# Performance work log

Hardware: AMD Instinct MI355X
Metric: run time of the kernel (lower is better)

The kernel has to match this reference:

```python
import jax, jax.numpy as jnp
import numpy as np

B, L, D, H = 2, 2048, 1024, 16
DH = D // H  # per-head dim = 64


def setup_inputs() -> dict:
    key = jax.random.key(0)
    ks = jax.random.split(key, 7)
    s = 1.0 / np.sqrt(D)
    x = jax.random.normal(ks[0], (B, L, D), dtype=jnp.float32)
    Wq = jax.random.normal(ks[1], (D, D), dtype=jnp.float32) * s
    bq = jax.random.normal(ks[2], (D,), dtype=jnp.float32) * s
    Wk = jax.random.normal(ks[3], (D, D), dtype=jnp.float32) * s
    bk = jax.random.normal(ks[4], (D,), dtype=jnp.float32) * s
    Wv = jax.random.normal(ks[5], (D, D), dtype=jnp.float32) * s
    bv = jax.random.normal(ks[6], (D,), dtype=jnp.float32) * s
    # strict upper-triangular causal mask; mask==1 means position is masked (-inf)
    atten_mask = jnp.triu(jnp.ones((L, L), dtype=jnp.int32), k=1)
    return {"x": x, "atten_mask": atten_mask, "Wq": Wq, "bq": bq,
            "Wk": Wk, "bk": bk, "Wv": Wv, "bv": bv}


def reference(x, atten_mask, Wq, bq, Wk, bk, Wv, bv):
    # nn.Linear: y = x @ W^T + b
    q = x @ Wq.T + bq  # [B,L,D]
    k = x @ Wk.T + bk
    v = x @ Wv.T + bv
    # contiguous split into heads == reshape to [B,L,H,DH]
    q = q.reshape(B, L, H, DH)
    k = k.reshape(B, L, H, DH)
    v = v.reshape(B, L, H, DH)
    scale = jnp.sqrt(jnp.float32(DH))
    scores = jnp.einsum('blhd,bmhd->bhlm', q, k) / scale  # [B,H,L,L]
    # torch.where(mask == 1, -inf, scores)
    scores = jnp.where(atten_mask[None, None] == 1, -jnp.inf, scores)
    attn = jax.nn.softmax(scores, axis=-1)
    out = jnp.einsum('bhlm,bmhd->blhd', attn, v)  # [B,L,H,DH]
    return out.reshape(B, L, D)  # concat heads along channel dim
```

## Files before the change

### kernel.cpp

```cpp
#include <hip/hip_runtime.h>
#include <hip/hip_bf16.h>

#define BDIM 2
#define LSEQ 2048
#define DMODEL 1024
#define NH 16
#define DHEAD 64
#define SP 72
#define CTS 136

typedef __bf16 bf16_t;
typedef __attribute__((ext_vector_type(8))) __bf16 bf16x8;
typedef __attribute__((ext_vector_type(4))) __bf16 bf16x4;
typedef __attribute__((ext_vector_type(2))) __bf16 bf16x2;
typedef __attribute__((ext_vector_type(4))) float f32x4;
typedef __attribute__((ext_vector_type(4))) int i32x4;

static __device__ __forceinline__ f32x4 mfma16(bf16x8 a, bf16x8 b, f32x4 c) {
    return __builtin_amdgcn_mfma_f32_16x16x32_bf16(a, b, c, 0, 0, 0);
}

static __device__ __forceinline__ void load_lds16(const bf16_t* g, void* l) {
    __builtin_amdgcn_global_load_lds(
        (const __attribute__((address_space(1))) void*)g,
        (__attribute__((address_space(3))) void*)l, 16, 0, 0);
}

__global__ void convert_all(
    const float* __restrict__ x,
    const float* __restrict__ Wq, const float* __restrict__ Wk, const float* __restrict__ Wv,
    const float* __restrict__ bq, const float* __restrict__ bk, const float* __restrict__ bv,
    bf16_t* __restrict__ cx,
    bf16_t* __restrict__ cWq, bf16_t* __restrict__ cWk, bf16_t* __restrict__ cWv,
    bf16_t* __restrict__ cbq, bf16_t* __restrict__ cbk, bf16_t* __restrict__ cbv,
    float SQ)
{
    const int blk = blockIdx.x;
    const float* src; bf16_t* dst; int base, cnt; float sc = 1.0f;
    if (blk < 1024)      { src = x;  dst = cx;  base = blk * 1024;          cnt = 1024; }
    else if (blk < 1280) { src = Wq; dst = cWq; base = (blk - 1024) * 1024; cnt = 1024; sc = SQ; }
    else if (blk < 1536) { src = Wk; dst = cWk; base = (blk - 1280) * 1024; cnt = 1024; }
    else if (blk < 1792) { src = Wv; dst = cWv; base = (blk - 1536) * 1024; cnt = 1024; }
    else if (blk == 1792){ src = bq; dst = cbq; base = 0; cnt = 256; sc = SQ; }
    else if (blk == 1793){ src = bk; dst = cbk; base = 0; cnt = 256; }
    else                 { src = bv; dst = cbv; base = 0; cnt = 256; }

    for (int i = base + threadIdx.x; i < base + cnt; i += 256) {
        f32x4 v = *(const f32x4*)(src + 4 * (size_t)i);
        bf16x4 o;
        o[0] = (bf16_t)(v[0] * sc); o[1] = (bf16_t)(v[1] * sc);
        o[2] = (bf16_t)(v[2] * sc); o[3] = (bf16_t)(v[3] * sc);
        *(bf16x4*)(dst + 4 * (size_t)i) = o;
    }
}

__global__ __launch_bounds__(512, 2) void qkv_gemm(
    const bf16_t* __restrict__ x,
    const bf16_t* __restrict__ W0, const bf16_t* __restrict__ W1, const bf16_t* __restrict__ W2,
    const bf16_t* __restrict__ b0, const bf16_t* __restrict__ b1, const bf16_t* __restrict__ b2,
    bf16_t* __restrict__ yq, bf16_t* __restrict__ yk, bf16_t* __restrict__ yvT)
{
    __shared__ alignas(16) bf16_t smem[65536];

    const int tid  = threadIdx.x;
    const int lane = tid & 63;
    const int w    = tid >> 6;
    const int quad = lane >> 4;
    const int n16  = lane & 15;
    const int swz  = n16 & 7;
    const int srow = lane >> 3;
    const int schnk = (lane & 7) ^ srow;

    const int s   = blockIdx.x;
    const int sem = ((s & 7) << 3) | (s >> 3);
    const int m0  = (sem >> 2) * 256;
    const int n0  = (sem & 3) * 256;
    const int z   = blockIdx.y;

    const bf16_t* W    = (z == 0) ? W0 : ((z == 1) ? W1 : W2);
    const bf16_t* bias = (z == 0) ? b0 : ((z == 1) ? b1 : b2);

    const int wm = (w >> 2) * 128;
    const int wn = (w & 3) * 64;

    const bf16_t* gA = x + (size_t)(m0 + w * 8 + srow) * DMODEL + schnk * 8;
    const bf16_t* gB = W + (size_t)(n0 + w * 8 + srow) * DMODEL + schnk * 8;

    f32x4 acc[8][4] = {};

    auto stageA = [&](int buf, int h, int kt) {
        bf16_t* d = smem + buf * 32768 + (h * 128 + w * 8) * 64;
        const bf16_t* src = gA + (size_t)(h * 128) * DMODEL + kt * 64;
        load_lds16(src, d);
        load_lds16(src + (size_t)64 * DMODEL, d + 64 * 64);
    };
    auto stageB = [&](int buf, int h, int kt) {
        bf16_t* d = smem + buf * 32768 + 16384 + (h * 128 + w * 8) * 64;
        const bf16_t* src = gB + (size_t)(h * 128) * DMODEL + kt * 64;
        load_lds16(src, d);
        load_lds16(src + (size_t)64 * DMODEL, d + 64 * 64);
    };

    stageA(0, 0, 0); stageA(0, 1, 0);
    stageB(0, 0, 0); stageB(0, 1, 0);
    stageB(1, 0, 1); stageB(1, 1, 1);
    asm volatile("s_waitcnt vmcnt(4)" ::: "memory");
    __builtin_amdgcn_s_barrier();

    for (int u = 0; u < 16; ++u) {
        const int buf = u & 1;
        const bf16_t* Ab = smem + buf * 32768;
        const bf16_t* Bb = Ab + 16384;

        bf16x8 bfr[4][2], af[2][2];
        #pragma unroll
        for (int nt = 0; nt < 4; ++nt) {
            const bf16_t* br = Bb + (wn + nt * 16 + n16) * 64;
            bfr[nt][0] = *(const bf16x8*)(br + ((quad    ) ^ swz) * 8);
            bfr[nt][1] = *(const bf16x8*)(br + ((quad + 4) ^ swz) * 8);
        }
        #pragma unroll
        for (int m2 = 0; m2 < 2; ++m2) {
            const bf16_t* ar = Ab + (wm + m2 * 16 + n16) * 64;
            af[m2][0] = *(const bf16x8*)(ar + ((quad    ) ^ swz) * 8);
            af[m2][1] = *(const bf16x8*)(ar + ((quad + 4) ^ swz) * 8);
        }
        if (u + 1 < 16) stageA(buf ^ 1, 0, u + 1);
        __builtin_amdgcn_s_barrier();
        asm volatile("s_waitcnt lgkmcnt(0)" ::: "memory");
        __builtin_amdgcn_sched_barrier(0);
        __builtin_amdgcn_s_setprio(1);
        #pragma unroll
        for (int m2 = 0; m2 < 2; ++m2)
            #pragma unroll
            for (int nt = 0; nt < 4; ++nt) {
                acc[m2][nt] = mfma16(af[m2][0], bfr[nt][0], acc[m2][nt]);
                acc[m2][nt] = mfma16(af[m2][1], bfr[nt][1], acc[m2][nt]);
            }
        __builtin_amdgcn_s_setprio(0);
        __builtin_amdgcn_s_barrier();

        #pragma unroll
        for (int q = 1; q < 4; ++q) {
            #pragma unroll
            for (int m2 = 0; m2 < 2; ++m2) {
                const bf16_t* ar = Ab + (wm + (2 * q + m2) * 16 + n16) * 64;
                af[m2][0] = *(const bf16x8*)(ar + ((quad    ) ^ swz) * 8);
                af[m2][1] = *(const bf16x8*)(ar + ((quad + 4) ^ swz) * 8);
            }
            if (q == 1) {
                if (u + 1 < 16) stageA(buf ^ 1, 1, u + 1);
                if (u + 2 < 16) stageB(buf, 0, u + 2);
            } else if (q == 2) {
                if (u + 2 < 16) stageB(buf, 1, u + 2);
            }
            __builtin_amdgcn_s_barrier();
            asm volatile("s_waitcnt lgkmcnt(0)" ::: "memory");
            __builtin_amdgcn_sched_barrier(0);
            __builtin_amdgcn_s_setprio(1);
            #pragma unroll
            for (int m2 = 0; m2 < 2; ++m2)
                #pragma unroll
                for (int nt = 0; nt < 4; ++nt) {
                    acc[2 * q + m2][nt] = mfma16(af[m2][0], bfr[nt][0], acc[2 * q + m2][nt]);
                    acc[2 * q + m2][nt] = mfma16(af[m2][1], bfr[nt][1], acc[2 * q + m2][nt]);
                }
            __builtin_amdgcn_s_setprio(0);
            if (q == 3) {
                if (u < 14) asm volatile("s_waitcnt vmcnt(4)" ::: "memory");
                else        asm volatile("s_waitcnt vmcnt(0)" ::: "memory");
            }
            __builtin_amdgcn_s_barrier();
        }
    }

    if (z < 2) {
        bf16_t* y = (z == 0) ? yq : yk;
        bf16_t* Ct = smem;
        #pragma unroll
        for (int hp = 0; hp < 2; ++hp) {
            if (((w & 3) >> 1) == hp) {
                #pragma unroll
                for (int nt = 0; nt < 4; ++nt) {
                    const int jc = (w & 1) * 64 + nt * 16 + n16;
                    const float bv = (float)bias[n0 + hp * 128 + jc];
                    #pragma unroll
                    for (int mt = 0; mt < 8; ++mt) {
                        const int rr = wm + mt * 16 + quad * 4;
                        #pragma unroll
                        for (int r = 0; r < 4; ++r)
                            Ct[(rr + r) * CTS + jc] = (bf16_t)(acc[mt][nt][r] + bv);
                    }
                }
            }
            __syncthreads();
            const int row = tid >> 1;
            const int seg = tid & 1;
            const int hh  = (n0 >> 6) + hp * 2 + seg;
            const int i   = m0 + row;
            const int bb  = i >> 11, ll = i & 2047;
            bf16_t* dst = &y[(((size_t)bb * NH + hh) * LSEQ + ll) * DHEAD];
            const bf16_t* srcr = &Ct[row * CTS + seg * 64];
            #pragma unroll
            for (int c = 0; c < 8; ++c)
                *(bf16x8*)(dst + c * 8) = *(const bf16x8*)(srcr + c * 8);
            __syncthreads();
        }
    } else {
        #pragma unroll
        for (int nt = 0; nt < 4; ++nt) {
            const int j = n0 + wn + nt * 16 + n16;
            const float bv = (float)bias[j];
            #pragma unroll
            for (int mt = 0; mt < 8; ++mt) {
                const int i0 = m0 + wm + mt * 16 + quad * 4;
                const int bb = i0 >> 11, l = i0 & 2047;
                bf16x4 pk;
                #pragma unroll
                for (int r = 0; r < 4; ++r) pk[r] = (bf16_t)(acc[mt][nt][r] + bv);
                *(bf16x4*)(&yvT[((size_t)bb * DMODEL + j) * LSEQ + l]) = pk;
            }
        }
    }
}

__global__ __launch_bounds__(256) void attn_fused(
    const bf16_t* __restrict__ qp,
    const bf16_t* __restrict__ kp,
    const bf16_t* __restrict__ vtp,
    float* __restrict__ out,
    float* __restrict__ Opart,
    float* __restrict__ ml)
{
    __shared__ alignas(16) bf16_t Ks[2][64 * 64];
    __shared__ alignas(16) bf16_t Vs[2][64 * 64];
    __shared__ alignas(16) bf16_t Pw[4][2][32 * SP];

    const int tid  = threadIdx.x;
    const int lane = tid & 63;
    const int w    = tid >> 6;
    const int quad = lane >> 4;
    const int n16  = lane & 15;
    const int lane3 = lane >> 3;
    const int lane7 = lane & 7;
    const int swz8  = (lane7 ^ lane3) * 8;
    const int swz   = n16 & 7;

    const int bh  = blockIdx.x;
    const int yy  = blockIdx.y;
    const int p   = yy & 7;
    const bool isA = (yy < 8);
    const int b = bh >> 4, h = bh & 15;
    const size_t hb = (size_t)bh * (LSEQ * DHEAD);

    float l_[2];
    f32x4 oacc[2][4];

    auto process = [&](int qt, int t0, int ntiles, bool maskTail) {
        int iqg[2];
        bf16x8 qb[2][2];
        #pragma unroll
        for (int g = 0; g < 2; ++g) {
            iqg[g] = qt * 128 + 32 * w + 16 * g + n16;
            const bf16_t* qq = qp + hb + (size_t)iqg[g] * DHEAD;
            qb[g][0] = *(const bf16x8*)(qq + quad * 8);
            qb[g][1] = *(const bf16x8*)(qq + 32 + quad * 8);
        }

        const bf16_t* gk = kp  + hb + (size_t)(t0 * 64 + 16 * w + lane3) * DHEAD + swz8;
        const bf16_t* gv = vtp + hb + (size_t)(16 * w + lane3) * LSEQ + t0 * 64 + swz8;

        int buf = 0;
        {
            char* lk = (char*)&Ks[0][0] + w * 2048;
            char* lv = (char*)&Vs[0][0] + w * 2048;
            load_lds16(gk,             lk);
            load_lds16(gk + 8 * DHEAD, lk + 1024);
            load_lds16(gv,             lv);
            load_lds16(gv + 8 * LSEQ,  lv + 1024);
            gk += 64 * DHEAD; gv += 64;
        }
        __syncthreads();

        for (int it = 0; it < ntiles; ++it) {
            if (it + 1 < ntiles) {
                char* lk = (char*)&Ks[buf ^ 1][0] + w * 2048;
                char* lv = (char*)&Vs[buf ^ 1][0] + w * 2048;
                load_lds16(gk,             lk);
                load_lds16(gk + 8 * DHEAD, lk + 1024);
                load_lds16(gv,             lv);
                load_lds16(gv + 8 * LSEQ,  lv + 1024);
                gk += 64 * DHEAD; gv += 64;
            }

            const bf16_t* kb = &Ks[buf][0];
            f32x4 s[2][4];
            #pragma unroll
            for (int t = 0; t < 4; ++t) {
                const bf16_t* krow = kb + (t * 16 + n16) * 64;
                bf16x8 k0v = *(const bf16x8*)(krow + ((quad    ) ^ swz) * 8);
                bf16x8 k1v = *(const bf16x8*)(krow + ((quad + 4) ^ swz) * 8);
                #pragma unroll
                for (int g = 0; g < 2; ++g) {
                    f32x4 z = {0.f, 0.f, 0.f, 0.f};
                    z = mfma16(k0v, qb[g][0], z);
                    z = mfma16(k1v, qb[g][1], z);
                    s[g][t] = z;
                }
            }

            if (maskTail && it >= ntiles - 2) {
                const int k0 = (t0 + it) * 64;
                #pragma unroll
                for (int g = 0; g < 2; ++g)
                    #pragma unroll
                    for (int t = 0; t < 4; ++t)
                        #pragma unroll
                        for (int r = 0; r < 4; ++r)
                            if (k0 + t * 16 + quad * 4 + r > iqg[g]) s[g][t][r] = -1e30f;
            }

            #pragma unroll
            for (int g = 0; g < 2; ++g) {
                bf16_t* pw = &Pw[w][buf][g * 16 * SP] + n16 * SP + quad * 4;
                float rs = 0.f;
                #pragma unroll
                for (int t = 0; t < 4; ++t) {
                    float p0 = __builtin_amdgcn_exp2f(s[g][t][0]);
                    float p1 = __builtin_amdgcn_exp2f(s[g][t][1]);
                    float p2 = __builtin_amdgcn_exp2f(s[g][t][2]);
                    float p3 = __builtin_amdgcn_exp2f(s[g][t][3]);
                    rs += (p0 + p1) + (p2 + p3);
                    bf16x4 pk;
                    pk[0] = (bf16_t)p0; pk[1] = (bf16_t)p1;
                    pk[2] = (bf16_t)p2; pk[3] = (bf16_t)p3;
                    *(bf16x4*)(pw + t * 16) = pk;
                }
                l_[g] += rs;
            }

            asm volatile("s_waitcnt lgkmcnt(0)" ::: "memory");

            const bf16_t* vbs = &Vs[buf][0];
            #pragma unroll
            for (int c = 0; c < 2; ++c) {
                bf16x8 pb0 = *(const bf16x8*)(&Pw[w][buf][0]       + n16 * SP + c * 32 + quad * 8);
                bf16x8 pb1 = *(const bf16x8*)(&Pw[w][buf][16 * SP] + n16 * SP + c * 32 + quad * 8);
                #pragma unroll
                for (int t = 0; t < 4; ++t) {
                    const bf16_t* vrow = vbs + (t * 16 + n16) * 64;
                    bf16x8 va = *(const bf16x8*)(vrow + ((quad + 4 * c) ^ swz) * 8);
                    oacc[0][t] = mfma16(va, pb0, oacc[0][t]);
                    oacc[1][t] = mfma16(va, pb1, oacc[1][t]);
                }
            }

            __syncthreads();
            buf ^= 1;
        }
    };

    auto zero_state = [&]() {
        #pragma unroll
        for (int g = 0; g < 2; ++g) {
            l_[g] = 0.f;
            #pragma unroll
            for (int t = 0; t < 4; ++t) { f32x4 zz = {0.f,0.f,0.f,0.f}; oacc[g][t] = zz; }
        }
    };

    auto store_partial = [&](int pidx) {
        #pragma unroll
        for (int g = 0; g < 2; ++g) {
            float ls = l_[g];
            ls += __shfl_xor(ls, 16, 64);
            ls += __shfl_xor(ls, 32, 64);
            const int row = 32 * w + 16 * g + n16;
            float* Ob = Opart + (size_t)pidx * (128 * 64) + row * 64;
            #pragma unroll
            for (int t = 0; t < 4; ++t)
                *(f32x4*)(Ob + t * 16 + quad * 4) = oacc[g][t];
            if (quad == 0) ml[(size_t)pidx * 128 + row] = ls;
        }
    };

    if (isA) {
        zero_state();
        process(p, 0, 2 * p + 2, true);
        #pragma unroll
        for (int g = 0; g < 2; ++g) {
            float ls = l_[g];
            ls += __shfl_xor(ls, 16, 64);
            ls += __shfl_xor(ls, 32, 64);
            const float inv = 1.0f / ls;
            const int iq = p * 128 + 32 * w + 16 * g + n16;
            float* orow = out + ((size_t)b * LSEQ + iq) * DMODEL + h * DHEAD;
            #pragma unroll
            for (int t = 0; t < 4; ++t) {
                f32x4 o;
                o[0] = oacc[g][t][0] * inv; o[1] = oacc[g][t][1] * inv;
                o[2] = oacc[g][t][2] * inv; o[3] = oacc[g][t][3] * inv;
                *(f32x4*)(orow + t * 16 + quad * 4) = o;
            }
        }
        zero_state();
        process(15 - p, 0, 15 - 2 * p, false);
        store_partial((bh * 8 + (7 - p)) * 2 + 0);
    } else {
        zero_state();
        process(15 - p, 15 - 2 * p, 17, true);
        store_partial((bh * 8 + (7 - p)) * 2 + 1);
    }
}

__global__ __launch_bounds__(256) void attn_combine(
    const float* __restrict__ Opart, const float* __restrict__ ml,
    float* __restrict__ out)
{
    const int bh = blockIdx.x;
    const int q8 = blockIdx.y;
    const int t  = threadIdx.x;
    const int row = t >> 1;
    const int dh0 = (t & 1) * 32;
    const int p0  = (bh * 8 + q8) * 2;
    const int b = bh >> 4, h = bh & 15;

    float l0 = ml[(size_t)p0 * 128 + row];
    float l1 = ml[(size_t)(p0 + 1) * 128 + row];
    float inv = 1.0f / (l0 + l1);

    const float* P0 = Opart + (size_t)p0 * (128 * 64) + row * 64 + dh0;
    const float* P1 = P0 + 128 * 64;
    float* orow = out + ((size_t)b * LSEQ + ((8 + q8) * 128 + row)) * DMODEL
                + h * DHEAD + dh0;
    #pragma unroll
    for (int c = 0; c < 8; ++c) {
        f32x4 o0 = *(const f32x4*)(P0 + 4 * c);
        f32x4 o1 = *(const f32x4*)(P1 + 4 * c);
        f32x4 o;
        o[0] = (o0[0] + o1[0]) * inv;
        o[1] = (o0[1] + o1[1]) * inv;
        o[2] = (o0[2] + o1[2]) * inv;
        o[3] = (o0[3] + o1[3]) * inv;
        *(f32x4*)(orow + 4 * c) = o;
    }
}

extern "C" void kernel_launch(void* const* d_in, const int* in_sizes, int n_in,
                              void* d_out, int out_size, void* d_ws, size_t ws_size,
                              hipStream_t stream)
{
    const float* x  = (const float*)d_in[0];
    const float* Wq = (const float*)d_in[2];
    const float* bq = (const float*)d_in[3];
    const float* Wk = (const float*)d_in[4];
    const float* bk = (const float*)d_in[5];
    const float* Wv = (const float*)d_in[6];
    const float* bv = (const float*)d_in[7];
    float* out = (float*)d_out;

    char* ws = (char*)d_ws;
    bf16_t* q   = (bf16_t*)(ws);
    bf16_t* k   = (bf16_t*)(ws + 8u  * 1024 * 1024);
    bf16_t* vT  = (bf16_t*)(ws + 16u * 1024 * 1024);
    bf16_t* cx  = (bf16_t*)(ws + 24u * 1024 * 1024);
    bf16_t* cWq = (bf16_t*)(ws + 32u * 1024 * 1024);
    bf16_t* cWk = (bf16_t*)(ws + 34u * 1024 * 1024);
    bf16_t* cWv = (bf16_t*)(ws + 36u * 1024 * 1024);
    bf16_t* cbq = (bf16_t*)(ws + 38u * 1024 * 1024);
    bf16_t* cbk = (bf16_t*)(ws + 38u * 1024 * 1024 + 4096);
    bf16_t* cbv = (bf16_t*)(ws + 38u * 1024 * 1024 + 8192);
    float*  mlp = (float*) (ws + 39u * 1024 * 1024);
    float*  Op  = (float*) (ws + 40u * 1024 * 1024);

    const float SQ = 0.125f * 1.44269504088896f;

    convert_all<<<1795, 256, 0, stream>>>(x, Wq, Wk, Wv, bq, bk, bv,
                                          cx, cWq, cWk, cWv, cbq, cbk, cbv, SQ);

    dim3 g1(64, 3, 1);
    qkv_gemm<<<g1, 512, 0, stream>>>(cx, cWq, cWk, cWv, cbq, cbk, cbv, q, k, vT);

    dim3 g2(BDIM * NH, 16, 1);
    attn_fused<<<g2, 256, 0, stream>>>(q, k, vT, out, Op, mlp);

    dim3 g3(BDIM * NH, 8, 1);
    attn_combine<<<g3, 256, 0, stream>>>(Op, mlp, out);
}
```

Baseline: 174.8 us.

## Software-pipeline A-fragment LDS reads and drop per-subtile barriers in QKV GEMM loop

Restructures the projection GEMM main loop so the next A-fragment LDS reads are prefetched into a second register set while the current MFMAs run. The four per-quarter workgroup barriers are replaced by a single barrier after the initial fragment loads and one at the end of the k-step. Both A stages for the next buffer are issued up front, and the B stage for u+2 is issued right after that barrier. This cuts barrier stalls and exposes LDS latency overlap with MFMA, at the cost of more VGPRs. It also risks hazards if stageB overwrites the current buffer while other waves are still reading it.

```diff
diff --git a/kernel.cpp b/kernel.cpp
--- a/kernel.cpp
+++ b/kernel.cpp
@@ -112,7 +112,7 @@
         const bf16_t* Ab = smem + buf * 32768;
         const bf16_t* Bb = Ab + 16384;
 
-        bf16x8 bfr[4][2], af[2][2];
+        bf16x8 bfr[4][2], af[2][2], afn[2][2];
         #pragma unroll
         for (int nt = 0; nt < 4; ++nt) {
             const bf16_t* br = Bb + (wn + nt * 16 + n16) * 64;
@@ -125,38 +125,24 @@
             af[m2][0] = *(const bf16x8*)(ar + ((quad    ) ^ swz) * 8);
             af[m2][1] = *(const bf16x8*)(ar + ((quad + 4) ^ swz) * 8);
         }
-        if (u + 1 < 16) stageA(buf ^ 1, 0, u + 1);
-        __builtin_amdgcn_s_barrier();
+        if (u + 1 < 16) { stageA(buf ^ 1, 0, u + 1); stageA(buf ^ 1, 1, u + 1); }
         asm volatile("s_waitcnt lgkmcnt(0)" ::: "memory");
         __builtin_amdgcn_sched_barrier(0);
-        __builtin_amdgcn_s_setprio(1);
-        #pragma unroll
-        for (int m2 = 0; m2 < 2; ++m2)
-            #pragma unroll
-            for (int nt = 0; nt < 4; ++nt) {
-                acc[m2][nt] = mfma16(af[m2][0], bfr[nt][0], acc[m2][nt]);
-                acc[m2][nt] = mfma16(af[m2][1], bfr[nt][1], acc[m2][nt]);
-            }
-        __builtin_amdgcn_s_setprio(0);
         __builtin_amdgcn_s_barrier();
-
-        #pragma unroll
-        for (int q = 1; q < 4; ++q) {
-            #pragma unroll
-            for (int m2 = 0; m2 < 2; ++m2) {
-                const bf16_t* ar = Ab + (wm + (2 * q + m2) * 16 + n16) * 64;
-                af[m2][0] = *(const bf16x8*)(ar + ((quad    ) ^ swz) * 8);
-                af[m2][1] = *(const bf16x8*)(ar + ((quad + 4) ^ swz) * 8);
-            }
-            if (q == 1) {
-                if (u + 1 < 16) stageA(buf ^ 1, 1, u + 1);
-                if (u + 2 < 16) stageB(buf, 0, u + 2);
-            } else if (q == 2) {
-                if (u + 2 < 16) stageB(buf, 1, u + 2);
-            }
-            __builtin_amdgcn_s_barrier();
-            asm volatile("s_waitcnt lgkmcnt(0)" ::: "memory");
-            __builtin_amdgcn_sched_barrier(0);
+        __builtin_amdgcn_sched_barrier(0);
+        if (u + 2 < 16) stageB(buf, 0, u + 2);
+
+        #pragma unroll
+        for (int q = 0; q < 4; ++q) {
+            if (q < 3) {
+                #pragma unroll
+                for (int m2 = 0; m2 < 2; ++m2) {
+                    const bf16_t* ar = Ab + (wm + (2 * (q + 1) + m2) * 16 + n16) * 64;
+                    afn[m2][0] = *(const bf16x8*)(ar + ((quad    ) ^ swz) * 8);
+                    afn[m2][1] = *(const bf16x8*)(ar + ((quad + 4) ^ swz) * 8);
+                }
+            }
+            if (q == 1 && u + 2 < 16) stageB(buf, 1, u + 2);
             __builtin_amdgcn_s_setprio(1);
             #pragma unroll
             for (int m2 = 0; m2 < 2; ++m2)
@@ -166,12 +152,18 @@
                     acc[2 * q + m2][nt] = mfma16(af[m2][1], bfr[nt][1], acc[2 * q + m2][nt]);
                 }
             __builtin_amdgcn_s_setprio(0);
-            if (q == 3) {
-                if (u < 14) asm volatile("s_waitcnt vmcnt(4)" ::: "memory");
-                else        asm volatile("s_waitcnt vmcnt(0)" ::: "memory");
-            }
-            __builtin_amdgcn_s_barrier();
-        }
+            if (q < 3) {
+                asm volatile("s_waitcnt lgkmcnt(0)" ::: "memory");
+                __builtin_amdgcn_sched_barrier(0);
+                #pragma unroll
+                for (int m2 = 0; m2 < 2; ++m2) {
+                    af[m2][0] = afn[m2][0]; af[m2][1] = afn[m2][1];
+                }
+            }
+        }
+        if (u < 14) asm volatile("s_waitcnt vmcnt(4)" ::: "memory");
+        else        asm volatile("s_waitcnt vmcnt(0)" ::: "memory");
+        __builtin_amdgcn_s_barrier();
     }
 
     if (z < 2) {
```

New measurement: 172.8 us. Within noise of the previous version (-1.1%).
